# Kernel optimization log

Hardware: AMD Instinct MI355X
Metric: run time of the kernel (lower is better)

Reference implementation:

```python
import jax, jax.numpy as jnp
import numpy as np

B, S, H = 16, 384, 768
DK, ESS, WHOLE = 64, 6, 8
HEADER = WHOLE + 1
NL_RGAT = 2


def _sinusoidal_pos(seq_len, dim):
    pos = np.arange(seq_len)[:, None]
    j = np.arange(dim)[None, :]
    enc = pos / np.power(10000.0, 2 * (j // 2) / dim)
    sent = dim // 2
    out = np.zeros((seq_len, dim), dtype=np.float32)
    out[:, :sent] = np.sin(enc[:, 0::2])
    out[:, sent:] = np.cos(enc[:, 1::2])
    return jnp.asarray(out)[None, None]  # [1,1,S,dim]


def _rope(pos, x):
    sin, cos = jnp.split(pos, 2, axis=-1)
    sin_pos = jnp.stack([sin, sin], -1).reshape(pos.shape)
    cos_pos = jnp.stack([cos, cos], -1).reshape(pos.shape)
    rot = jnp.stack([-x[..., 1::2], x[..., 0::2]], -1).reshape(x.shape)
    return x * cos_pos + rot * sin_pos


def _mlp(x, rep_w, rep_b, sc_w, sc_b):
    return jax.nn.relu(x @ rep_w.T + rep_b) @ sc_w.T + sc_b


def _heads(y, mask, n_heads):
    b, s = y.shape[:2]
    return (y * mask).reshape(b, s, n_heads, DK).transpose(0, 2, 1, 3)


def _shaking(M, rows, cols):
    # M: [B,nH,S,S] -> [B,P,nH]; upper triangle (incl diag), row-major
    return M[:, :, rows, cols].transpose(0, 2, 1)


def _layernorm(x, eps=1e-5):
    m = x.mean(-1, keepdims=True)
    v = ((x - m) ** 2).mean(-1, keepdims=True)
    return (x - m) * jax.lax.rsqrt(v + eps)


def setup_inputs() -> dict:
    key = jax.random.key(0)
    ks = jax.random.split(key, 32)
    n = lambda i, shape: jax.random.normal(ks[i], shape, dtype=jnp.float32) * 0.02
    ig = (H + DK * HEADER) // 2          # 672
    ip = (2 * H + DK * ESS) // 2          # 960
    return dict(
        seq_hiddens=jax.random.normal(ks[0], (B, S, H), dtype=jnp.float32),
        attention_mask=jnp.ones((B, S, 1), dtype=jnp.float32),
        wq4gt_w=n(1, (DK, H)), wq4gt_b=n(2, (DK,)),
        wk4gt_w=n(3, (DK, H)), wk4gt_b=n(4, (DK,)),
        wq4g_rep_w=n(5, (ig, H)), wq4g_rep_b=n(6, (ig,)),
        wq4g_sc_w=n(7, (DK * HEADER, ig)), wq4g_sc_b=n(8, (DK * HEADER,)),
        wk4g_rep_w=n(9, (ig, H)), wk4g_rep_b=n(10, (ig,)),
        wk4g_sc_w=n(11, (DK * HEADER, ig)), wk4g_sc_b=n(12, (DK * HEADER,)),
        rgat_w=n(13, (NL_RGAT, HEADER, H, H)),
        wq4t_w=n(14, (DK, 2 * H)), wq4t_b=n(15, (DK,)),
        wk4t_w=n(16, (DK, 2 * H)), wk4t_b=n(17, (DK,)),
        wq_rep_w=n(18, (ip, 2 * H)), wq_rep_b=n(19, (ip,)),
        wq_sc_w=n(20, (DK * ESS, ip)), wq_sc_b=n(21, (DK * ESS,)),
        wk_rep_w=n(22, (ip, 2 * H)), wk_rep_b=n(23, (ip,)),
        wk_sc_w=n(24, (DK * ESS, ip)), wk_sc_b=n(25, (DK * ESS,)),
    )


def reference(seq_hiddens, attention_mask,
              wq4gt_w, wq4gt_b, wk4gt_w, wk4gt_b,
              wq4g_rep_w, wq4g_rep_b, wq4g_sc_w, wq4g_sc_b,
              wk4g_rep_w, wk4g_rep_b, wk4g_sc_w, wk4g_sc_b,
              rgat_w,
              wq4t_w, wq4t_b, wk4t_w, wk4t_b,
              wq_rep_w, wq_rep_b, wq_sc_w, wq_sc_b,
              wk_rep_w, wk_rep_b, wk_sc_w, wk_sc_b):
    pos = _sinusoidal_pos(S, DK)
    rows, cols = np.triu_indices(S)
    inv = 1.0 / np.sqrt(DK).astype(np.float32)
    mask = attention_mask
    x = seq_hiddens

    # ----- graph layer (graph_stack_num = 1) -----
    tsq = _rope(pos, _heads(x @ wq4gt_w.T + wq4gt_b, mask, 1))
    tsk = _rope(pos, _heads(x @ wk4gt_w.T + wk4gt_b, mask, 1))
    thr_g = jax.nn.relu(_shaking(jnp.einsum('bhqd,bhkd->bhqk', tsq, tsk) * inv, rows, cols))

    q = _rope(pos, _heads(_mlp(x, wq4g_rep_w, wq4g_rep_b, wq4g_sc_w, wq4g_sc_b), mask, HEADER))
    k = _rope(pos, _heads(_mlp(x, wk4g_rep_w, wk4g_rep_b, wk4g_sc_w, wk4g_sc_b), mask, HEADER))
    score = jnp.einsum('bhqd,bhkd->bhqk', q, k) * inv  # [B,HEADER,S,S]
    sc_g = _shaking(score[:, :WHOLE], rows, cols)

    upper = jnp.triu(score, 1)
    diag = jnp.triu(score, 0) - upper
    att = upper + jnp.swapaxes(upper, -1, -2) + diag  # symmetric
    adj = jax.nn.softmax(att, -1) * (att != 0)

    feat = x
    for l in range(NL_RGAT):
        hr = jnp.einsum('bsh,roh->brso', feat, rgat_w[l])           # per-relation Linear (no bias)
        agg = jax.nn.relu(jnp.einsum('brst,brto->brso', adj, hr))   # adjacency bmm + ReLU
        feat = _layernorm(jax.nn.relu(agg.sum(1)) / HEADER)         # (dropout is eval-identity)

    # ----- prediction head -----
    inp = jnp.concatenate([seq_hiddens, feat], -1)  # [B,S,2H]
    tq = _rope(pos, _heads(inp @ wq4t_w.T + wq4t_b, mask, 1))
    tk = _rope(pos, _heads(inp @ wk4t_w.T + wk4t_b, mask, 1))
    thr_p = jax.nn.relu(_shaking(jnp.einsum('bhqd,bhkd->bhqk', tq, tk) * inv, rows, cols))

    qp = _rope(pos, _heads(_mlp(inp, wq_rep_w, wq_rep_b, wq_sc_w, wq_sc_b), mask, ESS))
    kp = _rope(pos, _heads(_mlp(inp, wk_rep_w, wk_rep_b, wk_sc_w, wk_sc_b), mask, ESS))
    sc_p = _shaking(jnp.einsum('bhqd,bhkd->bhqk', qp, kp) * inv, rows, cols)

    # concat all shaking outputs along last dim: [B, S(S+1)/2, ESS+1+WHOLE+1]
    return jnp.concatenate([sc_p, thr_p, sc_g, thr_g], -1)
```

## Files before the change

kernel.cpp:

```cpp
#include <hip/hip_runtime.h>
#include <math.h>

typedef unsigned short ushort_t;
typedef __attribute__((ext_vector_type(8))) short short8;
typedef __attribute__((ext_vector_type(4))) float f32x4;

constexpr int B = 16, S = 384, H = 768;
constexpr int BS = B * S;
constexpr long long PAIRS = (long long)S * (S + 1) / 2;
constexpr float INV = 0.125f;

__device__ __forceinline__ ushort_t f2bf(float f) {
  unsigned int u = __float_as_uint(f);
  u += 0x7FFF + ((u >> 16) & 1);
  return (ushort_t)(u >> 16);
}
__device__ __forceinline__ float bf2f(ushort_t u) {
  return __uint_as_float(((unsigned int)u) << 16);
}

__device__ __forceinline__ void glds16(const ushort_t* g, ushort_t* l) {
  __builtin_amdgcn_global_load_lds(
      (const __attribute__((address_space(1))) unsigned int*)g,
      (__attribute__((address_space(3))) unsigned int*)l, 16, 0, 0);
}

__global__ void rope_table_kernel(float* tab) {
  int s = blockIdx.x, i = threadIdx.x;
  double ang = (double)s / pow(10000.0, (double)i / 32.0);
  tab[s * 64 + 2 * i]     = (float)cos(ang);
  tab[s * 64 + 2 * i + 1] = (float)sin(ang);
}

constexpr int NJOBS = 14;
struct CvtJobs {
  const float* src[NJOBS];
  ushort_t* dst[NJOBS];
  int n_real[NJOBS];
  int n_tot[NJOBS];
  int blk_off[NJOBS + 1];
};
__global__ __launch_bounds__(256) void cvt_jobs_kernel(CvtJobs J) {
  int blk = blockIdx.x;
  int j = 0;
  while (j < NJOBS - 1 && blk >= J.blk_off[j + 1]) ++j;
  int i4 = (blk - J.blk_off[j]) * 256 + threadIdx.x;
  if (i4 * 4 >= J.n_tot[j]) return;
  ushort4 o;
  if (i4 * 4 < J.n_real[j]) {
    float4 v = ((const float4*)J.src[j])[i4];
    o = make_ushort4(f2bf(v.x), f2bf(v.y), f2bf(v.z), f2bf(v.w));
  } else {
    o = make_ushort4(0, 0, 0, 0);
  }
  ((ushort4*)J.dst[j])[i4] = o;
}

__global__ __launch_bounds__(256) void bias_concat_kernel(
    const float* g_repq, const float* g_repk, const float* g_gtq, const float* g_gtk,
    const float* p_repq, const float* p_repk, const float* p_gtq, const float* p_gtk,
    const float* g_scq, const float* g_sck, const float* p_scq, const float* p_sck,
    float* bqkg, float* bqkp, float* bscg, float* bscp) {
  int t = blockIdx.x * blockDim.x + threadIdx.x;
  if (t < 1472)
    bqkg[t] = t < 672 ? g_repq[t] : t < 1344 ? g_repk[t - 672]
            : t < 1408 ? g_gtq[t - 1344] : g_gtk[t - 1408];
  if (t < 2048)
    bqkp[t] = t < 960 ? p_repq[t] : t < 1920 ? p_repk[t - 960]
            : t < 1984 ? p_gtq[t - 1920] : p_gtk[t - 1984];
  if (t < 1152) bscg[t] = t < 576 ? g_scq[t] : g_sck[t - 576];
  if (t < 768)  bscp[t] = t < 384 ? p_scq[t] : p_sck[t - 384];
}

template <int ACT, int CMODE, int SWZ>
__global__ __launch_bounds__(256) void gemm_nt_mfma(
    const ushort_t* __restrict__ A, const ushort_t* __restrict__ W,
    const float* __restrict__ bias, void* __restrict__ Cv,
    ushort_t* __restrict__ pl, ushort_t* __restrict__ qd,
    ushort_t* __restrict__ kd, int cbase, int nsplit,
    int N, int K, int lda, int ldw, int ldc, float alpha, int nh,
    long long sAb, long long sAh, long long sWb, long long sWh,
    long long sCb, long long sCh,
    const float* __restrict__ mask, const float* __restrict__ tab, int biasN) {
  constexpr int SHSZ = (CMODE == 2) ? 17408 : 16384;
  __shared__ __align__(16) ushort_t SH[SHSZ];
  int bx = blockIdx.x, by = blockIdx.y, bz = blockIdx.z;
  if (SWZ) {
    const int nx = gridDim.x, ny = gridDim.y;
    const int nwg = nx * ny * gridDim.z;
    const int hw = bx + nx * (by + ny * bz);
    int l = (hw & 7) * (nwg >> 3) + (hw >> 3);
    const int pz = l / (nx * ny);
    int l2 = l - pz * (nx * ny);
    const int GM = 8;
    const int band = l2 / (GM * nx);
    const int rem = l2 - band * (GM * nx);
    const int gm = (ny - band * GM < GM) ? (ny - band * GM) : GM;
    bx = rem / gm;
    by = band * GM + (rem - bx * gm);
    bz = pz;
  }
  const int zb = bz / nh, zh = bz - zb * nh;
  A += zb * sAb + zh * sAh;
  W += zb * sWb + zh * sWh;
  const int t = threadIdx.x;
  const int m0 = by * 128, n0 = bx * 128;
  const int lane = t & 63, wid = t >> 6;
  const int wr = wid >> 1, wc = wid & 1;
  const int lrow = lane & 15, lk = lane >> 4;
  const int srow = t >> 2, sch = (t & 3) * 8;
  const ushort_t* Ag = A + (size_t)(m0 + srow) * lda + sch;
  const ushort_t* Wg = W + (size_t)(n0 + srow) * ldw + sch;
  const size_t a64 = (size_t)64 * lda, w64 = (size_t)64 * ldw;

  f32x4 acc[4][4];
#pragma unroll
  for (int i = 0; i < 4; ++i)
#pragma unroll
    for (int j = 0; j < 4; ++j) acc[i][j] = (f32x4){0.f, 0.f, 0.f, 0.f};

  auto stage = [&](int k0, int buf) {
    const int ao = buf * 4096, bo = 8192 + buf * 4096;
    glds16(Ag + k0, &SH[ao + t * 8]);
    glds16(Ag + k0 + a64, &SH[ao + 2048 + t * 8]);
    glds16(Wg + k0, &SH[bo + t * 8]);
    glds16(Wg + k0 + w64, &SH[bo + 2048 + t * 8]);
  };

  const int nk = K >> 5;
  stage(0, 0);
  for (int s = 0; s < nk; ++s) {
    __syncthreads();
    if (s + 1 < nk) stage((s + 1) << 5, (s + 1) & 1);
    const int ao = (s & 1) * 4096, bo = 8192 + (s & 1) * 4096;
    short8 av[4], bv[4];
#pragma unroll
    for (int i = 0; i < 4; ++i) {
      av[i] = *(const short8*)&SH[ao + (wr * 64 + i * 16 + lrow) * 32 + lk * 8];
      bv[i] = *(const short8*)&SH[bo + (wc * 64 + i * 16 + lrow) * 32 + lk * 8];
    }
#pragma unroll
    for (int i = 0; i < 4; ++i)
#pragma unroll
      for (int j = 0; j < 4; ++j)
        acc[i][j] = __builtin_amdgcn_mfma_f32_16x16x32_bf16(av[i], bv[j],
                                                            acc[i][j], 0, 0, 0);
  }

  if (CMODE == 2) {
    __syncthreads();
    const int bb = m0 / S;
    ushort_t* Cb = (ushort_t*)Cv + (size_t)bb * sCb;
    const int s_base = m0 - bb * S;
#pragma unroll
    for (int i = 0; i < 4; ++i) {
      const int sl = wr * 64 + i * 16 + lk * 4;
#pragma unroll
      for (int j = 0; j < 4; ++j) {
        const int nl = wc * 64 + j * 16 + lrow;
        ushort4 o = make_ushort4(f2bf(acc[i][j][0]), f2bf(acc[i][j][1]),
                                 f2bf(acc[i][j][2]), f2bf(acc[i][j][3]));
        *(ushort4*)&SH[nl * 136 + sl] = o;
      }
    }
    __syncthreads();
#pragma unroll
    for (int it = 0; it < 8; ++it) {
      const int row = it * 16 + wid * 4 + lk;
      ushort_t* dst = Cb + (size_t)(n0 + row) * ldc + s_base + lrow * 8;
      *(short8*)dst = *(const short8*)&SH[row * 136 + lrow * 8];
    }
  } else if (CMODE == 3) {
    ushort_t* plc = pl + ((size_t)(cbase + zh) * B + zb) * PAIRS;
#pragma unroll
    for (int j = 0; j < 4; ++j) {
      const int n = n0 + wc * 64 + j * 16 + lrow;
#pragma unroll
      for (int i = 0; i < 4; ++i) {
#pragma unroll
        for (int e = 0; e < 4; ++e) {
          const int m = m0 + wr * 64 + i * 16 + lk * 4 + e;
          if (n >= m) {
            long long p = (long long)m * S - (long long)m * (m - 1) / 2 + (n - m);
            float v = alpha * acc[i][j][e];
            if (ACT == 1) v = fmaxf(v, 0.f);
            plc[p] = f2bf(v);
          }
        }
      }
    }
  } else if (CMODE == 4) {
    ushort_t* Cu = (ushort_t*)Cv + zb * sCb + zh * sCh;
    ushort_t* plc = pl + ((size_t)(cbase + zh) * B + zb) * PAIRS;
#pragma unroll
    for (int j = 0; j < 4; ++j) {
      const int n = n0 + wc * 64 + j * 16 + lrow;
#pragma unroll
      for (int i = 0; i < 4; ++i) {
#pragma unroll
        for (int e = 0; e < 4; ++e) {
          const int m = m0 + wr * 64 + i * 16 + lk * 4 + e;
          float v = alpha * acc[i][j][e];
          ushort_t vb = f2bf(v);
          Cu[(size_t)m * ldc + n] = vb;
          if (zh < 8 && n >= m) {
            long long p = (long long)m * S - (long long)m * (m - 1) / 2 + (n - m);
            plc[p] = vb;
          }
        }
      }
    }
  } else if (CMODE == 5) {
    ushort_t* Cq = qd + (size_t)zh * sCh;
    const float* bz = bias + (size_t)zh * biasN;
#pragma unroll
    for (int j = 0; j < 4; ++j) {
      const int n = n0 + wc * 64 + j * 16 + lrow;
      const float vb = (n < N) ? bz[n] : 0.f;
      const int d = n & 63;
      const int ti = d & ~1;
#pragma unroll
      for (int i = 0; i < 4; ++i) {
#pragma unroll
        for (int e = 0; e < 4; ++e) {
          const int m = m0 + wr * 64 + i * 16 + lk * 4 + e;
          const int s = m % S;
          float v = (n < N) ? (acc[i][j][e] + vb) : 0.f;
          float pv = __shfl_xor(v, 1);
          float c = tab[s * 64 + ti], sn = tab[s * 64 + ti + 1];
          float o = (d & 1) ? (v * c + pv * sn) : (v * c - pv * sn);
          o *= mask[m];
          if (n < N) Cq[(size_t)m * ldc + n] = f2bf(o);
        }
      }
    }
  } else if (CMODE == 6) {
    ushort_t* Cu = (ushort_t*)Cv;
#pragma unroll
    for (int j = 0; j < 4; ++j) {
      const int n = n0 + wc * 64 + j * 16 + lrow;
      const float vb = (n < N) ? bias[n] : 0.f;
#pragma unroll
      for (int i = 0; i < 4; ++i) {
#pragma unroll
        for (int e = 0; e < 4; ++e) {
          const int m = m0 + wr * 64 + i * 16 + lk * 4 + e;
          float v = (n < N) ? (acc[i][j][e] + vb) : 0.f;
          float pv = __shfl_xor(v, 1);
          if (n < nsplit) {
            Cu[(size_t)m * ldc + n] = f2bf(fmaxf(v, 0.f));
          } else if (n < N) {
            const int d = n - nsplit;
            const int dd = d & 63;
            const int ti = dd & ~1;
            const int s = m % S;
            float c = tab[s * 64 + ti], sn = tab[s * 64 + ti + 1];
            float o = (dd & 1) ? (v * c + pv * sn) : (v * c - pv * sn);
            o *= mask[m];
            if (d < 64) qd[(size_t)m * 64 + dd] = f2bf(o);
            else        kd[(size_t)m * 64 + dd] = f2bf(o);
          }
        }
      }
    }
  }
}

__global__ __launch_bounds__(256) void adj_bmm_kernel(
    const ushort_t* __restrict__ adjb, const ushort_t* __restrict__ hrt,
    float* __restrict__ P0, float* __restrict__ P1, float* __restrict__ P2) {
  __shared__ __align__(16) ushort_t As[2][128 * 32];
  __shared__ __align__(16) ushort_t Bs[2][128 * 32];
  int bx = blockIdx.x, by = blockIdx.y, bz = blockIdx.z;
  {
    int nx = gridDim.x, ny = gridDim.y;
    int nwg = nx * ny * gridDim.z;
    int flat = bx + nx * (by + ny * bz);
    int l = (flat & 7) * (nwg >> 3) + (flat >> 3);
    bx = l % nx; l /= nx; by = l % ny; bz = l / ny;
  }
  const int b = bz / 3, rg = bz - b * 3;
  float* P = (rg == 0) ? P0 : (rg == 1) ? P1 : P2;
  const int t = threadIdx.x;
  const int m0 = by * 128, n0 = bx * 128;
  const int lane = t & 63, wid = t >> 6;
  const int wr = wid >> 1, wc = wid & 1;
  const int lrow = lane & 15, lk = lane >> 4;
  const int srow = t >> 2, sch = (t & 3) * 8;

  const ushort_t* adjA =
      adjb + ((size_t)(b * 9 + rg * 3) * S + m0 + srow) * S + sch;
  const ushort_t* hrA =
      hrt + ((size_t)(b * 9 + rg * 3) * H + n0 + srow) * S + sch;

  float mac[4][4][4];
#pragma unroll
  for (int i = 0; i < 4; ++i)
#pragma unroll
    for (int j = 0; j < 4; ++j)
#pragma unroll
      for (int e = 0; e < 4; ++e) mac[i][j][e] = 0.f;

  f32x4 acc[4][4];
#pragma unroll
  for (int i = 0; i < 4; ++i)
#pragma unroll
    for (int j = 0; j < 4; ++j) acc[i][j] = (f32x4){0.f, 0.f, 0.f, 0.f};

  auto stage = [&](int s, int buf) {
    const int rr = s / 12;
    const int k0 = (s - rr * 12) * 32;
    const ushort_t* Ag = adjA + (size_t)rr * S * S + k0;
    const ushort_t* Wg = hrA + (size_t)rr * H * S + k0;
    glds16(Ag, &As[buf][t * 8]);
    glds16(Ag + 64 * S, &As[buf][2048 + t * 8]);
    glds16(Wg, &Bs[buf][t * 8]);
    glds16(Wg + 64 * S, &Bs[buf][2048 + t * 8]);
  };

  stage(0, 0);
  for (int s = 0; s < 36; ++s) {
    __syncthreads();
    if (s + 1 < 36) stage(s + 1, (s + 1) & 1);
    const int buf = s & 1;
    short8 av[4], bv[4];
#pragma unroll
    for (int i = 0; i < 4; ++i) {
      av[i] = *(const short8*)&As[buf][(wr * 64 + i * 16 + lrow) * 32 + lk * 8];
      bv[i] = *(const short8*)&Bs[buf][(wc * 64 + i * 16 + lrow) * 32 + lk * 8];
    }
#pragma unroll
    for (int i = 0; i < 4; ++i)
#pragma unroll
      for (int j = 0; j < 4; ++j)
        acc[i][j] = __builtin_amdgcn_mfma_f32_16x16x32_bf16(av[i], bv[j],
                                                            acc[i][j], 0, 0, 0);
    if ((s % 12) == 11) {
#pragma unroll
      for (int i = 0; i < 4; ++i)
#pragma unroll
        for (int j = 0; j < 4; ++j) {
#pragma unroll
          for (int e = 0; e < 4; ++e)
            mac[i][j][e] += fmaxf(acc[i][j][e], 0.f);
          acc[i][j] = (f32x4){0.f, 0.f, 0.f, 0.f};
        }
    }
  }

#pragma unroll
  for (int i = 0; i < 4; ++i)
#pragma unroll
    for (int j = 0; j < 4; ++j)
#pragma unroll
      for (int e = 0; e < 4; ++e) {
        const int m = m0 + wr * 64 + i * 16 + lk * 4 + e;
        const int n = n0 + wc * 64 + j * 16 + lrow;
        P[((size_t)b * S + m) * H + n] = mac[i][j][e];
      }
}

__global__ __launch_bounds__(256) void sym_transpose_kernel(ushort_t* __restrict__ Mt) {
  __shared__ ushort_t T[32][33];
  int tp = blockIdx.x;
  int ti = 0;
  { int rem = tp, left = 12;
    while (rem >= left) { rem -= left; ++ti; --left; }
    tp = rem; }
  const int tj = ti + tp;
  ushort_t* base = Mt + (size_t)blockIdx.y * S * S;
  const int r = threadIdx.x >> 5, c = threadIdx.x & 31;
#pragma unroll
  for (int k = 0; k < 4; ++k)
    T[r + 8 * k][c] = base[(size_t)(ti * 32 + r + 8 * k) * S + tj * 32 + c];
  __syncthreads();
  if (ti == tj) {
#pragma unroll
    for (int k = 0; k < 4; ++k)
      if ((r + 8 * k) > c)
        base[(size_t)(ti * 32 + r + 8 * k) * S + tj * 32 + c] = T[c][r + 8 * k];
  } else {
#pragma unroll
    for (int k = 0; k < 4; ++k)
      base[(size_t)(tj * 32 + r + 8 * k) * S + ti * 32 + c] = T[c][r + 8 * k];
  }
}

__global__ __launch_bounds__(128) void softmax_mask_kernel(
    const ushort_t* __restrict__ Mt, ushort_t* __restrict__ adjb) {
  __shared__ float red[128];
  int row = blockIdx.x;
  const ushort_t* r = Mt + (size_t)row * S;
  ushort_t* o = adjb + (size_t)row * S;
  int t = threadIdx.x;
  float v[3];
  float mx = -INFINITY;
#pragma unroll
  for (int q = 0; q < 3; ++q) { v[q] = bf2f(r[t + q * 128]); mx = fmaxf(mx, v[q]); }
  red[t] = mx; __syncthreads();
  for (int off = 64; off > 0; off >>= 1) {
    if (t < off) red[t] = fmaxf(red[t], red[t + off]);
    __syncthreads();
  }
  mx = red[0]; __syncthreads();
  float e[3], s = 0.f;
#pragma unroll
  for (int q = 0; q < 3; ++q) { e[q] = expf(v[q] - mx); s += e[q]; }
  red[t] = s; __syncthreads();
  for (int off = 64; off > 0; off >>= 1) {
    if (t < off) red[t] += red[t + off];
    __syncthreads();
  }
  float invs = 1.f / red[0];
#pragma unroll
  for (int q = 0; q < 3; ++q)
    o[t + q * 128] = f2bf((v[q] != 0.f) ? e[q] * invs : 0.f);
}

__global__ __launch_bounds__(256) void ln_finalize_kernel(
    const float* __restrict__ P0, const float* __restrict__ P1,
    const float* __restrict__ P2, ushort_t* __restrict__ inp) {
  __shared__ float red[256];
  int row = blockIdx.x;
  const size_t base = (size_t)row * H;
  ushort_t* fb = inp + (size_t)row * (2 * H) + H;
  int t = threadIdx.x;
  float v[3];
  float s = 0.f;
#pragma unroll
  for (int q = 0; q < 3; ++q) {
    size_t ix = base + t + q * 256;
    v[q] = (P0[ix] + P1[ix] + P2[ix]) / 9.0f;
    s += v[q];
  }
  red[t] = s; __syncthreads();
  for (int off = 128; off > 0; off >>= 1) {
    if (t < off) red[t] += red[t + off];
    __syncthreads();
  }
  float mean = red[0] / (float)H; __syncthreads();
  float s2 = 0.f;
#pragma unroll
  for (int q = 0; q < 3; ++q) { float d = v[q] - mean; s2 += d * d; }
  red[t] = s2; __syncthreads();
  for (int off = 128; off > 0; off >>= 1) {
    if (t < off) red[t] += red[t + off];
    __syncthreads();
  }
  float var = red[0] / (float)H;
  float rs = rsqrtf(var + 1e-5f);
#pragma unroll
  for (int q = 0; q < 3; ++q)
    fb[t + q * 256] = f2bf((v[q] - mean) * rs);
}

__global__ __launch_bounds__(256) void copyx_kernel(
    const ushort_t* __restrict__ xb, ushort_t* __restrict__ inp) {
  int idx = blockIdx.x * 256 + threadIdx.x;
  if (idx >= BS * (H / 8)) return;
  int bs = idx / (H / 8), c8 = idx - bs * (H / 8);
  ((short8*)inp)[(size_t)bs * (2 * H / 8) + c8] = ((const short8*)xb)[idx];
}

__global__ __launch_bounds__(256) void gather16_kernel(
    const ushort_t* __restrict__ plA, const ushort_t* __restrict__ plB,
    float* __restrict__ out) {
  int idx = blockIdx.x * 256 + threadIdx.x;
  if (idx >= (int)(B * PAIRS)) return;
  const size_t PLN = (size_t)B * PAIRS;
  float v[16];
#pragma unroll
  for (int ch = 0; ch < 7; ++ch)  v[ch] = bf2f(plA[(size_t)ch * PLN + idx]);
#pragma unroll
  for (int ch = 7; ch < 16; ++ch) v[ch] = bf2f(plB[(size_t)(ch - 7) * PLN + idx]);
  float4* dst = (float4*)(out + (size_t)idx * 16);
#pragma unroll
  for (int q = 0; q < 4; ++q)
    dst[q] = make_float4(v[4 * q], v[4 * q + 1], v[4 * q + 2], v[4 * q + 3]);
}

extern "C" void kernel_launch(void* const* d_in, const int* in_sizes, int n_in,
                              void* d_out, int out_size, void* d_ws, size_t ws_size,
                              hipStream_t stream) {
  (void)in_sizes; (void)n_in; (void)out_size; (void)ws_size;
  const float* x          = (const float*)d_in[0];
  const float* mask       = (const float*)d_in[1];
  const float* wq4gt_w    = (const float*)d_in[2];
  const float* wq4gt_b    = (const float*)d_in[3];
  const float* wk4gt_w    = (const float*)d_in[4];
  const float* wk4gt_b    = (const float*)d_in[5];
  const float* wq4g_rep_w = (const float*)d_in[6];
  const float* wq4g_rep_b = (const float*)d_in[7];
  const float* wq4g_sc_w  = (const float*)d_in[8];
  const float* wq4g_sc_b  = (const float*)d_in[9];
  const float* wk4g_rep_w = (const float*)d_in[10];
  const float* wk4g_rep_b = (const float*)d_in[11];
  const float* wk4g_sc_w  = (const float*)d_in[12];
  const float* wk4g_sc_b  = (const float*)d_in[13];
  const float* rgat_w     = (const float*)d_in[14];
  const float* wq4t_w     = (const float*)d_in[15];
  const float* wq4t_b     = (const float*)d_in[16];
  const float* wk4t_w     = (const float*)d_in[17];
  const float* wk4t_b     = (const float*)d_in[18];
  const float* wq_rep_w   = (const float*)d_in[19];
  const float* wq_rep_b   = (const float*)d_in[20];
  const float* wq_sc_w    = (const float*)d_in[21];
  const float* wq_sc_b    = (const float*)d_in[22];
  const float* wk_rep_w   = (const float*)d_in[23];
  const float* wk_rep_b   = (const float*)d_in[24];
  const float* wk_sc_w    = (const float*)d_in[25];
  const float* wk_sc_b    = (const float*)d_in[26];
  float* out = (float*)d_out;

  char* wsb = (char*)d_ws;
  size_t off = 0;
  auto af = [&](size_t n) { float* p = (float*)(wsb + off);
                            off += ((n * 4 + 255) & ~(size_t)255); return p; };
  auto au = [&](size_t n) { ushort_t* p = (ushort_t*)(wsb + off);
                            off += ((n * 2 + 255) & ~(size_t)255); return p; };

  float* t_rope = af(24576);
  float* t_scg  = af((size_t)B * 9 * S * S);
  float* t_acc  = af((size_t)BS * H);
  ushort_t* xb    = au((size_t)BS * H);
  ushort_t* inpb  = au((size_t)BS * 2 * H);
  ushort_t* repb  = au((size_t)BS * 1920);
  ushort_t* qb    = au((size_t)BS * 576);
  ushort_t* kb    = au((size_t)BS * 576);
  ushort_t* adjb  = au((size_t)B * 9 * S * S);
  ushort_t* plB   = au((size_t)9 * B * PAIRS);
  ushort_t* wqkg  = au(1179648);
  ushort_t* wqkp  = au(3145728);
  ushort_t* wq4g_scb = au(430080);
  ushort_t* wk4g_scb = au(430080);
  ushort_t* wq_scb   = au(368640);
  ushort_t* wk_scb   = au(368640);
  ushort_t* rgatb    = au(10616832);
  float* bqkg = af(1472);
  float* bqkp = af(2048);
  float* bscg = af(1152);
  float* bscp = af(768);

  ushort_t* scg_u = (ushort_t*)t_scg;
  ushort_t* hr_t  = (ushort_t*)t_scg;
  ushort_t* plA   = rgatb;
  float* P0 = t_acc;
  float* P1 = (float*)repb;
  float* P2 = (float*)inpb;

  rope_table_kernel<<<S, 32, 0, stream>>>(t_rope);

  {
    CvtJobs J;
    const float* srcs[NJOBS] = {wq4g_rep_w, wk4g_rep_w, wq4gt_w, wk4gt_w,
                                wq_rep_w, wk_rep_w, wq4t_w, wk4t_w,
                                wq4g_sc_w, wk4g_sc_w, wq_sc_w, wk_sc_w,
                                rgat_w, x};
    ushort_t* dsts[NJOBS] = {wqkg, wqkg + 516096, wqkg + 1032192, wqkg + 1081344,
                             wqkp, wqkp + 1474560, wqkp + 2949120, wqkp + 3047424,
                             wq4g_scb, wk4g_scb, wq_scb, wk_scb,
                             rgatb, xb};
    int nreal[NJOBS] = {516096, 516096, 49152, 49152,
                        1474560, 1474560, 98304, 98304,
                        387072, 387072, 368640, 368640,
                        10616832, 4718592};
    int ntot[NJOBS]  = {516096, 516096, 49152, 98304,
                        1474560, 1474560, 98304, 98304,
                        430080, 430080, 368640, 368640,
                        10616832, 4718592};
    int acc_blk = 0;
    for (int j = 0; j < NJOBS; ++j) {
      J.src[j] = srcs[j]; J.dst[j] = dsts[j];
      J.n_real[j] = nreal[j]; J.n_tot[j] = ntot[j];
      J.blk_off[j] = acc_blk;
      acc_blk += (ntot[j] + 1023) / 1024;
    }
    J.blk_off[NJOBS] = acc_blk;
    cvt_jobs_kernel<<<acc_blk, 256, 0, stream>>>(J);
  }
  bias_concat_kernel<<<8, 256, 0, stream>>>(
      wq4g_rep_b, wk4g_rep_b, wq4gt_b, wk4gt_b,
      wq_rep_b, wk_rep_b, wq4t_b, wk4t_b,
      wq4g_sc_b, wk4g_sc_b, wq_sc_b, wk_sc_b,
      bqkg, bqkp, bscg, bscp);

  gemm_nt_mfma<0, 6, 1><<<dim3(12, 48, 1), 256, 0, stream>>>(
      xb, wqkg, bqkg, repb, nullptr, qb, kb, 0, 1344,
      1472, 768, 768, 768, 1344, 1.f, 1, 0, 0, 0, 0, 0, 0,
      mask, t_rope, 0);
  gemm_nt_mfma<1, 3, 1><<<dim3(3, 3, B), 256, 0, stream>>>(
      qb, kb, nullptr, nullptr, plB, nullptr, nullptr, 8, 0,
      S, 64, 64, 64, 0, INV, 1,
      (long long)S * 64, 0, (long long)S * 64, 0, 0, 0,
      nullptr, nullptr, 0);

  gemm_nt_mfma<0, 5, 1><<<dim3(5, 48, 2), 256, 0, stream>>>(
      repb, wq4g_scb, bscg, nullptr, nullptr, qb, nullptr, 0, 0,
      576, 672, 1344, 672, 576, 1.f, 2,
      0, 672, 0, 430080, 0, (long long)BS * 576,
      mask, t_rope, 576);
  gemm_nt_mfma<0, 4, 1><<<dim3(3, 3, B * 9), 256, 0, stream>>>(
      qb, kb, nullptr, scg_u, plB, nullptr, nullptr, 0, 0,
      S, 64, 576, 576, S, INV, 9,
      (long long)S * 576, 64, (long long)S * 576, 64,
      (long long)9 * S * S, (long long)S * S,
      nullptr, nullptr, 0);
  sym_transpose_kernel<<<dim3(78, B * 9), 256, 0, stream>>>(scg_u);
  softmax_mask_kernel<<<B * 9 * S, 128, 0, stream>>>(scg_u, adjb);

  for (int l = 0; l < 2; ++l) {
    const ushort_t* fsrc = (l == 0) ? xb : inpb + H;
    const int flda = (l == 0) ? H : 2 * H;
    gemm_nt_mfma<0, 2, 1><<<dim3(54, 48, 1), 256, 0, stream>>>(
        fsrc, rgatb + (size_t)l * 9 * H * H, nullptr, hr_t, nullptr, nullptr,
        nullptr, 0, 0,
        9 * H, H, flda, H, S, 1.f, 1, 0, 0, 0, 0, (long long)9 * H * S, 0,
        nullptr, nullptr, 0);
    adj_bmm_kernel<<<dim3(6, 3, B * 3), 256, 0, stream>>>(adjb, hr_t, P0, P1, P2);
    ln_finalize_kernel<<<BS, 256, 0, stream>>>(P0, P1, P2, inpb);
  }
  copyx_kernel<<<(BS * (H / 8) + 255) / 256, 256, 0, stream>>>(xb, inpb);

  gemm_nt_mfma<0, 6, 1><<<dim3(16, 48, 1), 256, 0, stream>>>(
      inpb, wqkp, bqkp, repb, nullptr, qb, kb, 0, 1920,
      2048, 1536, 1536, 1536, 1920, 1.f, 1, 0, 0, 0, 0, 0, 0,
      mask, t_rope, 0);
  gemm_nt_mfma<1, 3, 1><<<dim3(3, 3, B), 256, 0, stream>>>(
      qb, kb, nullptr, nullptr, plA, nullptr, nullptr, 6, 0,
      S, 64, 64, 64, 0, INV, 1,
      (long long)S * 64, 0, (long long)S * 64, 0, 0, 0,
      nullptr, nullptr, 0);

  gemm_nt_mfma<0, 5, 1><<<dim3(3, 48, 2), 256, 0, stream>>>(
      repb, wq_scb, bscp, nullptr, nullptr, qb, nullptr, 0, 0,
      384, 960, 1920, 960, 384, 1.f, 2,
      0, 960, 0, 368640, 0, (long long)BS * 384,
      mask, t_rope, 384);
  gemm_nt_mfma<0, 3, 1><<<dim3(3, 3, B * 6), 256, 0, stream>>>(
      qb, qb + (size_t)BS * 384, nullptr, nullptr, plA, nullptr, nullptr, 0, 0,
      S, 64, 384, 384, 0, INV, 6,
      (long long)S * 384, 64, (long long)S * 384, 64, 0, 0,
      nullptr, nullptr, 0);

  gather16_kernel<<<(int)((B * PAIRS + 255) / 256), 256, 0, stream>>>(plA, plB, out);
}
```

Measured before the change: 655.0 us.

## Compute only upper-triangular score tiles, fuse symmetric transpose, swap RGAT GEMM operands

```diff
diff --git a/kernel.cpp b/kernel.cpp
--- a/kernel.cpp
+++ b/kernel.cpp
@@ -82,7 +82,7 @@
     long long sAb, long long sAh, long long sWb, long long sWh,
     long long sCb, long long sCh,
     const float* __restrict__ mask, const float* __restrict__ tab, int biasN) {
-  constexpr int SHSZ = (CMODE == 2) ? 17408 : 16384;
+  constexpr int SHSZ = (CMODE == 8) ? 17408 : 16384;
   __shared__ __align__(16) ushort_t SH[SHSZ];
   int bx = blockIdx.x, by = blockIdx.y, bz = blockIdx.z;
   if (SWZ) {
@@ -104,7 +104,14 @@
   A += zb * sAb + zh * sAh;
   W += zb * sWb + zh * sWh;
   const int t = threadIdx.x;
-  const int m0 = by * 128, n0 = bx * 128;
+  int m0, n0;
+  if (CMODE == 3 || CMODE == 8) {
+    const int ti = (bx < 3) ? 0 : (bx < 5 ? 1 : 2);
+    const int tj = (bx < 3) ? bx : (bx < 5 ? bx - 2 : 2);
+    m0 = ti * 128; n0 = tj * 128;
+  } else {
+    m0 = by * 128; n0 = bx * 128;
+  }
   const int lane = t & 63, wid = t >> 6;
   const int wr = wid >> 1, wc = wid & 1;
   const int lrow = lane & 15, lk = lane >> 4;
@@ -147,30 +154,7 @@
                                                             acc[i][j], 0, 0, 0);
   }
 
-  if (CMODE == 2) {
-    __syncthreads();
-    const int bb = m0 / S;
-    ushort_t* Cb = (ushort_t*)Cv + (size_t)bb * sCb;
-    const int s_base = m0 - bb * S;
-#pragma unroll
-    for (int i = 0; i < 4; ++i) {
-      const int sl = wr * 64 + i * 16 + lk * 4;
-#pragma unroll
-      for (int j = 0; j < 4; ++j) {
-        const int nl = wc * 64 + j * 16 + lrow;
-        ushort4 o = make_ushort4(f2bf(acc[i][j][0]), f2bf(acc[i][j][1]),
-                                 f2bf(acc[i][j][2]), f2bf(acc[i][j][3]));
-        *(ushort4*)&SH[nl * 136 + sl] = o;
-      }
-    }
-    __syncthreads();
-#pragma unroll
-    for (int it = 0; it < 8; ++it) {
-      const int row = it * 16 + wid * 4 + lk;
-      ushort_t* dst = Cb + (size_t)(n0 + row) * ldc + s_base + lrow * 8;
-      *(short8*)dst = *(const short8*)&SH[row * 136 + lrow * 8];
-    }
-  } else if (CMODE == 3) {
+  if (CMODE == 3) {
     ushort_t* plc = pl + ((size_t)(cbase + zh) * B + zb) * PAIRS;
 #pragma unroll
     for (int j = 0; j < 4; ++j) {
@@ -189,36 +173,15 @@
         }
       }
     }
-  } else if (CMODE == 4) {
-    ushort_t* Cu = (ushort_t*)Cv + zb * sCb + zh * sCh;
-    ushort_t* plc = pl + ((size_t)(cbase + zh) * B + zb) * PAIRS;
+  } else if (CMODE == 5) {
+    ushort_t* Cq = qd + (size_t)zh * sCh;
+    const float* bz2 = bias + (size_t)zh * biasN;
 #pragma unroll
     for (int j = 0; j < 4; ++j) {
       const int n = n0 + wc * 64 + j * 16 + lrow;
-#pragma unroll
-      for (int i = 0; i < 4; ++i) {
-#pragma unroll
-        for (int e = 0; e < 4; ++e) {
-          const int m = m0 + wr * 64 + i * 16 + lk * 4 + e;
-          float v = alpha * acc[i][j][e];
-          ushort_t vb = f2bf(v);
-          Cu[(size_t)m * ldc + n] = vb;
-          if (zh < 8 && n >= m) {
-            long long p = (long long)m * S - (long long)m * (m - 1) / 2 + (n - m);
-            plc[p] = vb;
-          }
-        }
-      }
-    }
-  } else if (CMODE == 5) {
-    ushort_t* Cq = qd + (size_t)zh * sCh;
-    const float* bz = bias + (size_t)zh * biasN;
-#pragma unroll
-    for (int j = 0; j < 4; ++j) {
-      const int n = n0 + wc * 64 + j * 16 + lrow;
-      const float vb = (n < N) ? bz[n] : 0.f;
+      const float vb = (n < N) ? bz2[n] : 0.f;
       const int d = n & 63;
-      const int ti = d & ~1;
+      const int ti2 = d & ~1;
 #pragma unroll
       for (int i = 0; i < 4; ++i) {
 #pragma unroll
@@ -227,7 +190,7 @@
           const int s = m % S;
           float v = (n < N) ? (acc[i][j][e] + vb) : 0.f;
           float pv = __shfl_xor(v, 1);
-          float c = tab[s * 64 + ti], sn = tab[s * 64 + ti + 1];
+          float c = tab[s * 64 + ti2], sn = tab[s * 64 + ti2 + 1];
           float o = (d & 1) ? (v * c + pv * sn) : (v * c - pv * sn);
           o *= mask[m];
           if (n < N) Cq[(size_t)m * ldc + n] = f2bf(o);
@@ -252,15 +215,83 @@
           } else if (n < N) {
             const int d = n - nsplit;
             const int dd = d & 63;
-            const int ti = dd & ~1;
+            const int ti2 = dd & ~1;
             const int s = m % S;
-            float c = tab[s * 64 + ti], sn = tab[s * 64 + ti + 1];
+            float c = tab[s * 64 + ti2], sn = tab[s * 64 + ti2 + 1];
             float o = (dd & 1) ? (v * c + pv * sn) : (v * c - pv * sn);
             o *= mask[m];
             if (d < 64) qd[(size_t)m * 64 + dd] = f2bf(o);
             else        kd[(size_t)m * 64 + dd] = f2bf(o);
           }
         }
+      }
+    }
+  } else if (CMODE == 7) {
+    const int b = n0 / S;
+    ushort_t* Cb = (ushort_t*)Cv + (size_t)b * 9 * H * S;
+#pragma unroll
+    for (int j = 0; j < 4; ++j) {
+      const int n = n0 + wc * 64 + j * 16 + lrow;
+      const int s = n - b * S;
+#pragma unroll
+      for (int i = 0; i < 4; ++i) {
+#pragma unroll
+        for (int e = 0; e < 4; ++e) {
+          const int m = m0 + wr * 64 + i * 16 + lk * 4 + e;
+          Cb[(size_t)m * S + s] = f2bf(acc[i][j][e]);
+        }
+      }
+    }
+  } else if (CMODE == 8) {
+    ushort_t* Cu = (ushort_t*)Cv + zb * sCb + zh * sCh;
+    ushort_t* plc = pl + ((size_t)(cbase + zh) * B + zb) * PAIRS;
+    const bool diag = (m0 == n0);
+#pragma unroll
+    for (int j = 0; j < 4; ++j) {
+      const int n = n0 + wc * 64 + j * 16 + lrow;
+#pragma unroll
+      for (int i = 0; i < 4; ++i) {
+#pragma unroll
+        for (int e = 0; e < 4; ++e) {
+          const int m = m0 + wr * 64 + i * 16 + lk * 4 + e;
+          float v = alpha * acc[i][j][e];
+          ushort_t vb = f2bf(v);
+          if (!diag || n >= m) Cu[(size_t)m * ldc + n] = vb;
+          if (zh < 8 && n >= m) {
+            long long p = (long long)m * S - (long long)m * (m - 1) / 2 + (n - m);
+            plc[p] = vb;
+          }
+        }
+      }
+    }
+    __syncthreads();
+#pragma unroll
+    for (int i = 0; i < 4; ++i) {
+      const int sl = wr * 64 + i * 16 + lk * 4;
+#pragma unroll
+      for (int j = 0; j < 4; ++j) {
+        const int nl = wc * 64 + j * 16 + lrow;
+        ushort4 o4 = make_ushort4(f2bf(alpha * acc[i][j][0]),
+                                  f2bf(alpha * acc[i][j][1]),
+                                  f2bf(alpha * acc[i][j][2]),
+                                  f2bf(alpha * acc[i][j][3]));
+        *(ushort4*)&SH[nl * 136 + sl] = o4;
+      }
+    }
+    __syncthreads();
+#pragma unroll
+    for (int it = 0; it < 8; ++it) {
+      const int rowN = it * 16 + wid * 4 + lk;
+      const int colM = lrow * 8;
+      if (!diag) {
+        *(short8*)&Cu[(size_t)(n0 + rowN) * ldc + m0 + colM] =
+            *(const short8*)&SH[rowN * 136 + colM];
+      } else {
+#pragma unroll
+        for (int q = 0; q < 8; ++q)
+          if (rowN > colM + q)
+            Cu[(size_t)(n0 + rowN) * ldc + m0 + colM + q] =
+                SH[rowN * 136 + colM + q];
       }
     }
   }
@@ -360,32 +391,6 @@
       }
 }
 
-__global__ __launch_bounds__(256) void sym_transpose_kernel(ushort_t* __restrict__ Mt) {
-  __shared__ ushort_t T[32][33];
-  int tp = blockIdx.x;
-  int ti = 0;
-  { int rem = tp, left = 12;
-    while (rem >= left) { rem -= left; ++ti; --left; }
-    tp = rem; }
-  const int tj = ti + tp;
-  ushort_t* base = Mt + (size_t)blockIdx.y * S * S;
-  const int r = threadIdx.x >> 5, c = threadIdx.x & 31;
-#pragma unroll
-  for (int k = 0; k < 4; ++k)
-    T[r + 8 * k][c] = base[(size_t)(ti * 32 + r + 8 * k) * S + tj * 32 + c];
-  __syncthreads();
-  if (ti == tj) {
-#pragma unroll
-    for (int k = 0; k < 4; ++k)
-      if ((r + 8 * k) > c)
-        base[(size_t)(ti * 32 + r + 8 * k) * S + tj * 32 + c] = T[c][r + 8 * k];
-  } else {
-#pragma unroll
-    for (int k = 0; k < 4; ++k)
-      base[(size_t)(tj * 32 + r + 8 * k) * S + ti * 32 + c] = T[c][r + 8 * k];
-  }
-}
-
 __global__ __launch_bounds__(128) void softmax_mask_kernel(
     const ushort_t* __restrict__ Mt, ushort_t* __restrict__ adjb) {
   __shared__ float red[128];
@@ -393,28 +398,39 @@
   const ushort_t* r = Mt + (size_t)row * S;
   ushort_t* o = adjb + (size_t)row * S;
   int t = threadIdx.x;
-  float v[3];
+  const bool act = t < 96;
+  float v[4];
   float mx = -INFINITY;
-#pragma unroll
-  for (int q = 0; q < 3; ++q) { v[q] = bf2f(r[t + q * 128]); mx = fmaxf(mx, v[q]); }
+  if (act) {
+    ushort4 u = ((const ushort4*)r)[t];
+    v[0] = bf2f(u.x); v[1] = bf2f(u.y); v[2] = bf2f(u.z); v[3] = bf2f(u.w);
+    mx = fmaxf(fmaxf(v[0], v[1]), fmaxf(v[2], v[3]));
+  }
   red[t] = mx; __syncthreads();
-  for (int off = 64; off > 0; off >>= 1) {
-    if (t < off) red[t] = fmaxf(red[t], red[t + off]);
+  for (int off2 = 64; off2 > 0; off2 >>= 1) {
+    if (t < off2) red[t] = fmaxf(red[t], red[t + off2]);
     __syncthreads();
   }
   mx = red[0]; __syncthreads();
-  float e[3], s = 0.f;
-#pragma unroll
-  for (int q = 0; q < 3; ++q) { e[q] = expf(v[q] - mx); s += e[q]; }
+  float e4[4], s = 0.f;
+  if (act) {
+#pragma unroll
+    for (int q = 0; q < 4; ++q) { e4[q] = expf(v[q] - mx); s += e4[q]; }
+  }
   red[t] = s; __syncthreads();
-  for (int off = 64; off > 0; off >>= 1) {
-    if (t < off) red[t] += red[t + off];
+  for (int off2 = 64; off2 > 0; off2 >>= 1) {
+    if (t < off2) red[t] += red[t + off2];
     __syncthreads();
   }
   float invs = 1.f / red[0];
-#pragma unroll
-  for (int q = 0; q < 3; ++q)
-    o[t + q * 128] = f2bf((v[q] != 0.f) ? e[q] * invs : 0.f);
+  if (act) {
+    ushort4 ou;
+    ou.x = f2bf((v[0] != 0.f) ? e4[0] * invs : 0.f);
+    ou.y = f2bf((v[1] != 0.f) ? e4[1] * invs : 0.f);
+    ou.z = f2bf((v[2] != 0.f) ? e4[2] * invs : 0.f);
+    ou.w = f2bf((v[3] != 0.f) ? e4[3] * invs : 0.f);
+    ((ushort4*)o)[t] = ou;
+  }
 }
 
 __global__ __launch_bounds__(256) void ln_finalize_kernel(
@@ -434,8 +450,8 @@
     s += v[q];
   }
   red[t] = s; __syncthreads();
-  for (int off = 128; off > 0; off >>= 1) {
-    if (t < off) red[t] += red[t + off];
+  for (int off2 = 128; off2 > 0; off2 >>= 1) {
+    if (t < off2) red[t] += red[t + off2];
     __syncthreads();
   }
   float mean = red[0] / (float)H; __syncthreads();
@@ -443,8 +459,8 @@
 #pragma unroll
   for (int q = 0; q < 3; ++q) { float d = v[q] - mean; s2 += d * d; }
   red[t] = s2; __syncthreads();
-  for (int off = 128; off > 0; off >>= 1) {
-    if (t < off) red[t] += red[t + off];
+  for (int off2 = 128; off2 > 0; off2 >>= 1) {
+    if (t < off2) red[t] += red[t + off2];
     __syncthreads();
   }
   float var = red[0] / (float)H;
@@ -588,7 +604,7 @@
       xb, wqkg, bqkg, repb, nullptr, qb, kb, 0, 1344,
       1472, 768, 768, 768, 1344, 1.f, 1, 0, 0, 0, 0, 0, 0,
       mask, t_rope, 0);
-  gemm_nt_mfma<1, 3, 1><<<dim3(3, 3, B), 256, 0, stream>>>(
+  gemm_nt_mfma<1, 3, 1><<<dim3(6, 1, B), 256, 0, stream>>>(
       qb, kb, nullptr, nullptr, plB, nullptr, nullptr, 8, 0,
       S, 64, 64, 64, 0, INV, 1,
       (long long)S * 64, 0, (long long)S * 64, 0, 0, 0,
@@ -599,22 +615,21 @@
       576, 672, 1344, 672, 576, 1.f, 2,
       0, 672, 0, 430080, 0, (long long)BS * 576,
       mask, t_rope, 576);
-  gemm_nt_mfma<0, 4, 1><<<dim3(3, 3, B * 9), 256, 0, stream>>>(
+  gemm_nt_mfma<0, 8, 1><<<dim3(6, 1, B * 9), 256, 0, stream>>>(
       qb, kb, nullptr, scg_u, plB, nullptr, nullptr, 0, 0,
       S, 64, 576, 576, S, INV, 9,
       (long long)S * 576, 64, (long long)S * 576, 64,
       (long long)9 * S * S, (long long)S * S,
       nullptr, nullptr, 0);
-  sym_transpose_kernel<<<dim3(78, B * 9), 256, 0, stream>>>(scg_u);
   softmax_mask_kernel<<<B * 9 * S, 128, 0, stream>>>(scg_u, adjb);
 
   for (int l = 0; l < 2; ++l) {
     const ushort_t* fsrc = (l == 0) ? xb : inpb + H;
     const int flda = (l == 0) ? H : 2 * H;
-    gemm_nt_mfma<0, 2, 1><<<dim3(54, 48, 1), 256, 0, stream>>>(
-        fsrc, rgatb + (size_t)l * 9 * H * H, nullptr, hr_t, nullptr, nullptr,
+    gemm_nt_mfma<0, 7, 1><<<dim3(48, 54, 1), 256, 0, stream>>>(
+        rgatb + (size_t)l * 9 * H * H, fsrc, nullptr, hr_t, nullptr, nullptr,
         nullptr, 0, 0,
-        9 * H, H, flda, H, S, 1.f, 1, 0, 0, 0, 0, (long long)9 * H * S, 0,
+        BS, H, H, flda, S, 1.f, 1, 0, 0, 0, 0, 0, 0,
         nullptr, nullptr, 0);
     adj_bmm_kernel<<<dim3(6, 3, B * 3), 256, 0, stream>>>(adjb, hr_t, P0, P1, P2);
     ln_finalize_kernel<<<BS, 256, 0, stream>>>(P0, P1, P2, inpb);
@@ -625,7 +640,7 @@
       inpb, wqkp, bqkp, repb, nullptr, qb, kb, 0, 1920,
       2048, 1536, 1536, 1536, 1920, 1.f, 1, 0, 0, 0, 0, 0, 0,
       mask, t_rope, 0);
-  gemm_nt_mfma<1, 3, 1><<<dim3(3, 3, B), 256, 0, stream>>>(
+  gemm_nt_mfma<1, 3, 1><<<dim3(6, 1, B), 256, 0, stream>>>(
       qb, kb, nullptr, nullptr, plA, nullptr, nullptr, 6, 0,
       S, 64, 64, 64, 0, INV, 1,
       (long long)S * 64, 0, (long long)S * 64, 0, 0, 0,
@@ -636,7 +651,7 @@
       384, 960, 1920, 960, 384, 1.f, 2,
       0, 960, 0, 368640, 0, (long long)BS * 384,
       mask, t_rope, 384);
-  gemm_nt_mfma<0, 3, 1><<<dim3(3, 3, B * 6), 256, 0, stream>>>(
+  gemm_nt_mfma<0, 3, 1><<<dim3(6, 1, B * 6), 256, 0, stream>>>(
       qb, qb + (size_t)BS * 384, nullptr, nullptr, plA, nullptr, nullptr, 0, 0,
       S, 64, 384, 384, 0, INV, 6,
       (long long)S * 384, 64, (long long)S * 384, 64, 0, 0,
```

Measured after the change: 664.7 us. About the same (+1.5%).
